# Performance work log

Hardware: AMD Instinct MI355X
Metric: run time of the kernel (lower is better)

The kernel has to match this reference:

```python
import jax, jax.numpy as jnp
import numpy as np

B, IN_F, OUT_F, K = 8192, 1024, 4096, 2
S = 64  # sqrt(OUT_F)


def setup_inputs() -> dict:
    key = jax.random.key(0)
    k1, k2, k3, k4 = jax.random.split(key, 4)
    x = jax.random.normal(k1, (B, IN_F), dtype=jnp.float32)
    y = jax.random.normal(k2, (B, OUT_F), dtype=jnp.float32)
    weight = jax.random.normal(k3, (OUT_F, IN_F), dtype=jnp.float32) * (1.0 / np.sqrt(IN_F))
    bias = jax.random.normal(k4, (OUT_F,), dtype=jnp.float32) * (1.0 / np.sqrt(IN_F))
    return {"x": x, "y": y, "weight": weight, "bias": bias}


def reference(x, y, weight, bias):
    # fused GEMM + bias + residual add epilogue
    out_lin = jnp.einsum('bk,nk->bn', x, weight) + bias + y  # (B, OUT_F)
    feat = out_lin.reshape(B, S, S)
    # AvgPool2d(kernel=K, stride=K)
    s_out = S // K
    pooled = feat.reshape(B, s_out, K, s_out, K).mean(axis=(2, 4))  # (B, s_out, s_out)
    # divide by global mean of the pooled map
    mean_val = pooled.mean()
    normed = pooled / mean_val
    return normed[:, None, :, :]  # (B, 1, s_out, s_out)
```

## Files before the change

### kernel.cpp

```cpp
#include <hip/hip_runtime.h>
#include <stdint.h>


#define KDIM 1024
#define NP   1024
#define BM 128
#define BN 128
#define BK 64

typedef __bf16 bf16x8 __attribute__((ext_vector_type(8)));
typedef float f32x4 __attribute__((ext_vector_type(4)));

__device__ __forceinline__ unsigned f2bf(float f) {
  union { float f; unsigned u; } v; v.f = f;
  unsigned r = v.u + 0x7fffu + ((v.u >> 16) & 1u);
  return r >> 16;
}

__device__ __forceinline__ void gload_lds16(const void* g, void* l) {
  __builtin_amdgcn_global_load_lds(
      (const __attribute__((address_space(1))) void*)g,
      (__attribute__((address_space(3))) void*)l, 16, 0, 0);
}

__global__ void k_prep(const float* __restrict__ x, const float* __restrict__ W,
                       const float* __restrict__ bias,
                       unsigned short* __restrict__ xb, unsigned short* __restrict__ wp,
                       float* __restrict__ biasp) {
  int b = blockIdx.x;
  int t = threadIdx.x;
  if (b < 4096) {
    int i = b * 256 + t;
    const float4* x4 = (const float4*)x;
    float4 a = x4[i * 2], c = x4[i * 2 + 1];
    uint4 o;
    o.x = f2bf(a.x) | (f2bf(a.y) << 16);
    o.y = f2bf(a.z) | (f2bf(a.w) << 16);
    o.z = f2bf(c.x) | (f2bf(c.y) << 16);
    o.w = f2bf(c.z) | (f2bf(c.w) << 16);
    ((uint4*)xb)[i] = o;
  } else {
    int o = b - 4096;
    int r0 = ((o >> 5) << 7) + ((o & 31) << 1);
    const float4* W4 = (const float4*)W;
    float4 w0 = W4[(r0) * 256 + t];
    float4 w1 = W4[(r0 + 1) * 256 + t];
    float4 w2 = W4[(r0 + 64) * 256 + t];
    float4 w3 = W4[(r0 + 65) * 256 + t];
    float ax = 0.25f * (w0.x + w1.x + w2.x + w3.x);
    float ay = 0.25f * (w0.y + w1.y + w2.y + w3.y);
    float az = 0.25f * (w0.z + w1.z + w2.z + w3.z);
    float aw = 0.25f * (w0.w + w1.w + w2.w + w3.w);
    uint2 pk;
    pk.x = f2bf(ax) | (f2bf(ay) << 16);
    pk.y = f2bf(az) | (f2bf(aw) << 16);
    ((uint2*)wp)[o * 256 + t] = pk;
    if (t == 0)
      biasp[o] = 0.25f * (bias[r0] + bias[r0 + 1] + bias[r0 + 64] + bias[r0 + 65]);
  }
}

__global__ __launch_bounds__(256) void k_gemm(
    const unsigned short* __restrict__ xb, const unsigned short* __restrict__ wp,
    const float* __restrict__ biasp, const float* __restrict__ y,
    float* __restrict__ out, float* __restrict__ partials) {
  __shared__ char smem[65536];

  int bid = blockIdx.x;
  int wg = (bid & 7) * 64 + (bid >> 3);
  int bm0 = (wg >> 3) * BM;
  int bn0 = (wg & 7) * BN;

  int tid = threadIdx.x;
  int lane = tid & 63;
  int wid = tid >> 6;
  int wr = wid >> 1, wc = wid & 1;

  f32x4 acc[4][4];
#pragma unroll
  for (int i = 0; i < 4; i++)
#pragma unroll
    for (int j = 0; j < 4; j++) acc[i][j] = (f32x4)0.0f;

  int srow = wid * 32 + (lane >> 3);
  int scol = (((lane & 7) ^ (lane >> 3)) << 3);
  const unsigned short* aSrc = xb + (size_t)(bm0 + srow) * KDIM + scol;
  const unsigned short* bSrc = wp + (size_t)(bn0 + srow) * KDIM + scol;
  int ldsOff = wid * 4096;

  int rbase = (lane & 15) * 128;
  int xorv = (lane & 7) << 4;
  int cb0 = (((lane >> 4) * 16)) ^ xorv;
  int cb1 = ((64 + (lane >> 4) * 16)) ^ xorv;

#define STAGE(buf, ks)                                                         \
  {                                                                            \
    int k0 = (ks) * BK;                                                        \
    char* ab = smem + (buf) * 32768 + ldsOff;                                  \
    char* bb = smem + (buf) * 32768 + 16384 + ldsOff;                          \
    _Pragma("unroll")                                                          \
    for (int i = 0; i < 4; ++i) {                                              \
      gload_lds16(aSrc + (size_t)i * 8 * KDIM + k0, ab + i * 1024);            \
      gload_lds16(bSrc + (size_t)i * 8 * KDIM + k0, bb + i * 1024);            \
    }                                                                          \
  }

  STAGE(0, 0);
  for (int ks = 0; ks < 16; ++ks) {
    int cur = ks & 1;
    if (ks < 15) {
      STAGE(cur ^ 1, ks + 1);
      asm volatile("s_waitcnt vmcnt(8)" ::: "memory");
    } else {
      asm volatile("s_waitcnt vmcnt(0)" ::: "memory");
    }
    __builtin_amdgcn_s_barrier();
    asm volatile("" ::: "memory");
    const char* Ab = smem + cur * 32768;
    const char* Bb = Ab + 16384;
#pragma unroll
    for (int kk = 0; kk < 2; ++kk) {
      int cb = kk ? cb1 : cb0;
      bf16x8 af[4], bfr[4];
#pragma unroll
      for (int mi = 0; mi < 4; ++mi)
        af[mi] = *(const bf16x8*)(Ab + (wr * 64 + mi * 16) * 128 + rbase + cb);
#pragma unroll
      for (int ni = 0; ni < 4; ++ni)
        bfr[ni] = *(const bf16x8*)(Bb + (wc * 64 + ni * 16) * 128 + rbase + cb);
#pragma unroll
      for (int mi = 0; mi < 4; ++mi)
#pragma unroll
        for (int ni = 0; ni < 4; ++ni)
          acc[mi][ni] = __builtin_amdgcn_mfma_f32_16x16x32_bf16(af[mi], bfr[ni], acc[mi][ni], 0, 0, 0);
    }
    asm volatile("" ::: "memory");
    __builtin_amdgcn_s_barrier();
  }

  const float2* y2 = (const float2*)y;
  float tsum = 0.f;
  int r_l = (lane >> 4) * 4;
  int c_l = lane & 15;
#pragma unroll
  for (int mi = 0; mi < 4; ++mi) {
#pragma unroll
    for (int ni = 0; ni < 4; ++ni) {
      int col = bn0 + wc * 64 + ni * 16 + c_l;
      float bp = biasp[col];
      int y2base = ((col >> 5) << 6) + (col & 31);
#pragma unroll
      for (int j = 0; j < 4; ++j) {
        int row = bm0 + wr * 64 + mi * 16 + r_l + j;
        float2 u = y2[(size_t)row * 2048 + y2base];
        float2 v = y2[(size_t)row * 2048 + y2base + 32];
        float val = acc[mi][ni][j] + bp + 0.25f * (u.x + u.y + v.x + v.y);
        out[(size_t)row * NP + col] = val;
        tsum += val;
      }
    }
  }
#pragma unroll
  for (int off = 32; off > 0; off >>= 1) tsum += __shfl_down(tsum, off);
  float* ws4 = (float*)smem;
  __syncthreads();
  if (lane == 0) ws4[wid] = tsum;
  __syncthreads();
  if (tid == 0) partials[bid] = ws4[0] + ws4[1] + ws4[2] + ws4[3];
}

__global__ void k_reduce(const float* __restrict__ partials, float* __restrict__ invm) {
  __shared__ float s[256];
  int t = threadIdx.x;
  s[t] = partials[t] + partials[t + 256];
  __syncthreads();
  for (int off = 128; off > 0; off >>= 1) {
    if (t < off) s[t] += s[t + off];
    __syncthreads();
  }
  if (t == 0) invm[0] = 8388608.0f / s[0];
}

__global__ void k_norm(float* __restrict__ out, const float* __restrict__ invm) {
  int i = blockIdx.x * 256 + threadIdx.x;
  float inv = invm[0];
  float4* o4 = (float4*)out;
  float4 v = o4[i];
  v.x *= inv; v.y *= inv; v.z *= inv; v.w *= inv;
  o4[i] = v;
}

extern "C" void kernel_launch(void* const* d_in, const int* in_sizes, int n_in,
                              void* d_out, int out_size, void* d_ws, size_t ws_size,
                              hipStream_t stream) {
  (void)in_sizes; (void)n_in; (void)out_size; (void)ws_size;
  const float* x = (const float*)d_in[0];
  const float* y = (const float*)d_in[1];
  const float* W = (const float*)d_in[2];
  const float* bias = (const float*)d_in[3];
  float* out = (float*)d_out;

  char* ws = (char*)d_ws;
  unsigned short* xb = (unsigned short*)(ws);
  unsigned short* wp = (unsigned short*)(ws + 16777216);
  float* biasp = (float*)(ws + 16777216 + 2097152);
  float* partials = (float*)(ws + 16777216 + 2097152 + 4096);
  float* invm = (float*)(ws + 16777216 + 2097152 + 4096 + 2048);

  hipLaunchKernelGGL(k_prep, dim3(5120), dim3(256), 0, stream, x, W, bias, xb, wp, biasp);
  hipLaunchKernelGGL(k_gemm, dim3(512), dim3(256), 0, stream, xb, wp, biasp, y, out, partials);
  hipLaunchKernelGGL(k_reduce, dim3(1), dim3(256), 0, stream, partials, invm);
  hipLaunchKernelGGL(k_norm, dim3(8192), dim3(256), 0, stream, out, invm);
}
```

Before: 67.75 us.

## Fuse global mean reduction and normalization into GEMM via grid-wide atomic barrier

Each GEMM block keeps its epilogue values in registers and publishes its partial sum. It then increments a global counter and spins until all 512 blocks have arrived. Every block reduces all partials itself and writes the normalized output directly. This removes the reduce and normalize kernel launches and a full extra read and write of the output. It relies on all 512 blocks being co-resident (two per CU on 256 CUs); otherwise it hangs until the iteration cap, and it adds spin-wait latency and higher register pressure.

After: 137.4 us. +102.8%, slower.

```diff
diff --git a/kernel.cpp b/kernel.cpp
--- a/kernel.cpp
+++ b/kernel.cpp
@@ -7,6 +7,7 @@
 #define BM 128
 #define BN 128
 #define BK 64
+#define NBLK 512
 
 typedef __bf16 bf16x8 __attribute__((ext_vector_type(8)));
 typedef float f32x4 __attribute__((ext_vector_type(4)));
@@ -26,7 +27,7 @@
 __global__ void k_prep(const float* __restrict__ x, const float* __restrict__ W,
                        const float* __restrict__ bias,
                        unsigned short* __restrict__ xb, unsigned short* __restrict__ wp,
-                       float* __restrict__ biasp) {
+                       float* __restrict__ biasp, unsigned* __restrict__ counter) {
   int b = blockIdx.x;
   int t = threadIdx.x;
   if (b < 4096) {
@@ -39,6 +40,8 @@
     o.z = f2bf(c.x) | (f2bf(c.y) << 16);
     o.w = f2bf(c.z) | (f2bf(c.w) << 16);
     ((uint4*)xb)[i] = o;
+    if (b == 0 && t == 0)
+      __hip_atomic_store(counter, 0u, __ATOMIC_RELAXED, __HIP_MEMORY_SCOPE_AGENT);
   } else {
     int o = b - 4096;
     int r0 = ((o >> 5) << 7) + ((o & 31) << 1);
@@ -63,7 +66,8 @@
 __global__ __launch_bounds__(256) void k_gemm(
     const unsigned short* __restrict__ xb, const unsigned short* __restrict__ wp,
     const float* __restrict__ biasp, const float* __restrict__ y,
-    float* __restrict__ out, float* __restrict__ partials) {
+    float* __restrict__ out, float* __restrict__ partials,
+    unsigned* __restrict__ counter) {
   __shared__ char smem[65536];
 
   int bid = blockIdx.x;
@@ -155,39 +159,53 @@
         float2 u = y2[(size_t)row * 2048 + y2base];
         float2 v = y2[(size_t)row * 2048 + y2base + 32];
         float val = acc[mi][ni][j] + bp + 0.25f * (u.x + u.y + v.x + v.y);
-        out[(size_t)row * NP + col] = val;
+        acc[mi][ni][j] = val;
         tsum += val;
       }
     }
   }
 #pragma unroll
   for (int off = 32; off > 0; off >>= 1) tsum += __shfl_down(tsum, off);
-  float* ws4 = (float*)smem;
-  __syncthreads();
-  if (lane == 0) ws4[wid] = tsum;
-  __syncthreads();
-  if (tid == 0) partials[bid] = ws4[0] + ws4[1] + ws4[2] + ws4[3];
-}
-
-__global__ void k_reduce(const float* __restrict__ partials, float* __restrict__ invm) {
-  __shared__ float s[256];
-  int t = threadIdx.x;
-  s[t] = partials[t] + partials[t + 256];
-  __syncthreads();
+  float* sm = (float*)smem;
+  __syncthreads();
+  if (lane == 0) sm[wid] = tsum;
+  __syncthreads();
+
+  if (tid == 0) {
+    float p = sm[0] + sm[1] + sm[2] + sm[3];
+    __hip_atomic_store(&partials[bid], p, __ATOMIC_RELEASE, __HIP_MEMORY_SCOPE_AGENT);
+    __hip_atomic_fetch_add(counter, 1u, __ATOMIC_ACQ_REL, __HIP_MEMORY_SCOPE_AGENT);
+    for (long it = 0; it < (1L << 26); ++it) {
+      if (__hip_atomic_load(counter, __ATOMIC_ACQUIRE, __HIP_MEMORY_SCOPE_AGENT) >= NBLK) break;
+      __builtin_amdgcn_s_sleep(8);
+    }
+  }
+  __syncthreads();
+
+  float pv = __hip_atomic_load(&partials[tid], __ATOMIC_RELAXED, __HIP_MEMORY_SCOPE_AGENT) +
+             __hip_atomic_load(&partials[tid + 256], __ATOMIC_RELAXED, __HIP_MEMORY_SCOPE_AGENT);
+  __syncthreads();
+  sm[tid] = pv;
+  __syncthreads();
+#pragma unroll
   for (int off = 128; off > 0; off >>= 1) {
-    if (t < off) s[t] += s[t + off];
+    if (tid < off) sm[tid] += sm[tid + off];
     __syncthreads();
   }
-  if (t == 0) invm[0] = 8388608.0f / s[0];
-}
-
-__global__ void k_norm(float* __restrict__ out, const float* __restrict__ invm) {
-  int i = blockIdx.x * 256 + threadIdx.x;
-  float inv = invm[0];
-  float4* o4 = (float4*)out;
-  float4 v = o4[i];
-  v.x *= inv; v.y *= inv; v.z *= inv; v.w *= inv;
-  o4[i] = v;
+  float inv = 8388608.0f / sm[0];
+
+#pragma unroll
+  for (int mi = 0; mi < 4; ++mi) {
+#pragma unroll
+    for (int ni = 0; ni < 4; ++ni) {
+      int col = bn0 + wc * 64 + ni * 16 + c_l;
+#pragma unroll
+      for (int j = 0; j < 4; ++j) {
+        int row = bm0 + wr * 64 + mi * 16 + r_l + j;
+        out[(size_t)row * NP + col] = acc[mi][ni][j] * inv;
+      }
+    }
+  }
 }
 
 extern "C" void kernel_launch(void* const* d_in, const int* in_sizes, int n_in,
@@ -205,10 +223,8 @@
   unsigned short* wp = (unsigned short*)(ws + 16777216);
   float* biasp = (float*)(ws + 16777216 + 2097152);
   float* partials = (float*)(ws + 16777216 + 2097152 + 4096);
-  float* invm = (float*)(ws + 16777216 + 2097152 + 4096 + 2048);
-
-  hipLaunchKernelGGL(k_prep, dim3(5120), dim3(256), 0, stream, x, W, bias, xb, wp, biasp);
-  hipLaunchKernelGGL(k_gemm, dim3(512), dim3(256), 0, stream, xb, wp, biasp, y, out, partials);
-  hipLaunchKernelGGL(k_reduce, dim3(1), dim3(256), 0, stream, partials, invm);
-  hipLaunchKernelGGL(k_norm, dim3(8192), dim3(256), 0, stream, out, invm);
-}
+  unsigned* counter = (unsigned*)(ws + 16777216 + 2097152 + 8192);
+
+  hipLaunchKernelGGL(k_prep, dim3(5120), dim3(256), 0, stream, x, W, bias, xb, wp, biasp, counter);
+  hipLaunchKernelGGL(k_gemm, dim3(512), dim3(256), 0, stream, xb, wp, biasp, y, out, partials, counter);
+}
```

## Enlarge GEMM tile to 256x128 with 8 waves and fold reduce into norm

Applied to the files above, without the earlier changes.

The GEMM block tile grows from 128x128 with 4 waves to 256x128 with 8 waves (512 threads), halving the grid to 256 blocks. Each block now reuses its B tile across more rows, and the LDS staging layout is adjusted to match. The separate single-block reduce kernel is removed, and every k_norm block now re-reduces the 256 partials itself. This saves one launch but makes each of the 8192 norm blocks do a redundant shared-memory reduction. The larger 96KB LDS footprint may also limit occupancy, and 256 blocks may underfill the GPU's CUs.

After: 69.99 us. 3.3% more time.

```diff
diff --git a/kernel.cpp b/kernel.cpp
--- a/kernel.cpp
+++ b/kernel.cpp
@@ -4,9 +4,10 @@
 
 #define KDIM 1024
 #define NP   1024
-#define BM 128
+#define BM 256
 #define BN 128
 #define BK 64
+#define NBLK 256
 
 typedef __bf16 bf16x8 __attribute__((ext_vector_type(8)));
 typedef float f32x4 __attribute__((ext_vector_type(4)));
@@ -60,14 +61,14 @@
   }
 }
 
-__global__ __launch_bounds__(256) void k_gemm(
+__global__ __launch_bounds__(512, 2) void k_gemm(
     const unsigned short* __restrict__ xb, const unsigned short* __restrict__ wp,
     const float* __restrict__ biasp, const float* __restrict__ y,
     float* __restrict__ out, float* __restrict__ partials) {
-  __shared__ char smem[65536];
+  __shared__ char smem[98304];
 
   int bid = blockIdx.x;
-  int wg = (bid & 7) * 64 + (bid >> 3);
+  int wg = (bid & 7) * 32 + (bid >> 3);
   int bm0 = (wg >> 3) * BM;
   int bn0 = (wg & 7) * BN;
 
@@ -82,11 +83,11 @@
 #pragma unroll
     for (int j = 0; j < 4; j++) acc[i][j] = (f32x4)0.0f;
 
-  int srow = wid * 32 + (lane >> 3);
+  int srow = tid >> 3;
   int scol = (((lane & 7) ^ (lane >> 3)) << 3);
   const unsigned short* aSrc = xb + (size_t)(bm0 + srow) * KDIM + scol;
   const unsigned short* bSrc = wp + (size_t)(bn0 + srow) * KDIM + scol;
-  int ldsOff = wid * 4096;
+  int ldsOff = wid * 1024;
 
   int rbase = (lane & 15) * 128;
   int xorv = (lane & 7) << 4;
@@ -96,13 +97,14 @@
 #define STAGE(buf, ks)                                                         \
   {                                                                            \
     int k0 = (ks) * BK;                                                        \
-    char* ab = smem + (buf) * 32768 + ldsOff;                                  \
-    char* bb = smem + (buf) * 32768 + 16384 + ldsOff;                          \
+    char* ab = smem + (buf) * 49152 + ldsOff;                                  \
+    char* bb = smem + (buf) * 49152 + 32768 + ldsOff;                          \
     _Pragma("unroll")                                                          \
-    for (int i = 0; i < 4; ++i) {                                              \
-      gload_lds16(aSrc + (size_t)i * 8 * KDIM + k0, ab + i * 1024);            \
-      gload_lds16(bSrc + (size_t)i * 8 * KDIM + k0, bb + i * 1024);            \
-    }                                                                          \
+    for (int i = 0; i < 4; ++i)                                                \
+      gload_lds16(aSrc + (size_t)i * 64 * KDIM + k0, ab + i * 8192);           \
+    _Pragma("unroll")                                                          \
+    for (int i = 0; i < 2; ++i)                                                \
+      gload_lds16(bSrc + (size_t)i * 64 * KDIM + k0, bb + i * 8192);           \
   }
 
   STAGE(0, 0);
@@ -110,14 +112,14 @@
     int cur = ks & 1;
     if (ks < 15) {
       STAGE(cur ^ 1, ks + 1);
-      asm volatile("s_waitcnt vmcnt(8)" ::: "memory");
+      asm volatile("s_waitcnt vmcnt(6)" ::: "memory");
     } else {
       asm volatile("s_waitcnt vmcnt(0)" ::: "memory");
     }
     __builtin_amdgcn_s_barrier();
     asm volatile("" ::: "memory");
-    const char* Ab = smem + cur * 32768;
-    const char* Bb = Ab + 16384;
+    const char* Ab = smem + cur * 49152;
+    const char* Bb = Ab + 32768;
 #pragma unroll
     for (int kk = 0; kk < 2; ++kk) {
       int cb = kk ? cb1 : cb0;
@@ -162,28 +164,27 @@
   }
 #pragma unroll
   for (int off = 32; off > 0; off >>= 1) tsum += __shfl_down(tsum, off);
-  float* ws4 = (float*)smem;
+  float* sm = (float*)smem;
   __syncthreads();
-  if (lane == 0) ws4[wid] = tsum;
+  if (lane == 0) sm[wid] = tsum;
   __syncthreads();
-  if (tid == 0) partials[bid] = ws4[0] + ws4[1] + ws4[2] + ws4[3];
-}
-
-__global__ void k_reduce(const float* __restrict__ partials, float* __restrict__ invm) {
+  if (tid == 0)
+    partials[bid] = ((sm[0] + sm[1]) + (sm[2] + sm[3])) +
+                    ((sm[4] + sm[5]) + (sm[6] + sm[7]));
+}
+
+__global__ void k_norm(float* __restrict__ out, const float* __restrict__ partials) {
   __shared__ float s[256];
   int t = threadIdx.x;
-  s[t] = partials[t] + partials[t + 256];
+  s[t] = partials[t];
   __syncthreads();
+#pragma unroll
   for (int off = 128; off > 0; off >>= 1) {
     if (t < off) s[t] += s[t + off];
     __syncthreads();
   }
-  if (t == 0) invm[0] = 8388608.0f / s[0];
-}
-
-__global__ void k_norm(float* __restrict__ out, const float* __restrict__ invm) {
-  int i = blockIdx.x * 256 + threadIdx.x;
-  float inv = invm[0];
+  float inv = 8388608.0f / s[0];
+  int i = blockIdx.x * 256 + t;
   float4* o4 = (float4*)out;
   float4 v = o4[i];
   v.x *= inv; v.y *= inv; v.z *= inv; v.w *= inv;
@@ -205,10 +206,8 @@
   unsigned short* wp = (unsigned short*)(ws + 16777216);
   float* biasp = (float*)(ws + 16777216 + 2097152);
   float* partials = (float*)(ws + 16777216 + 2097152 + 4096);
-  float* invm = (float*)(ws + 16777216 + 2097152 + 4096 + 2048);
 
   hipLaunchKernelGGL(k_prep, dim3(5120), dim3(256), 0, stream, x, W, bias, xb, wp, biasp);
-  hipLaunchKernelGGL(k_gemm, dim3(512), dim3(256), 0, stream, xb, wp, biasp, y, out, partials);
-  hipLaunchKernelGGL(k_reduce, dim3(1), dim3(256), 0, stream, partials, invm);
-  hipLaunchKernelGGL(k_norm, dim3(8192), dim3(256), 0, stream, out, invm);
-}
+  hipLaunchKernelGGL(k_gemm, dim3(NBLK), dim3(512), 0, stream, xb, wp, biasp, y, out, partials);
+  hipLaunchKernelGGL(k_norm, dim3(8192), dim3(256), 0, stream, out, partials);
+}
```
